# Performance work log

Hardware: AMD Instinct MI355X
Metric: run time of the kernel (lower is better)

The kernel has to match this reference:

```python
import jax, jax.numpy as jnp
import numpy as np

D = 1024
H = 16
HD = D // H

def setup_inputs() -> dict:
    key = jax.random.key(0)
    ks = jax.random.split(key, 6)
    tokens = jax.random.normal(ks[0], (2, 2048, D), dtype=jnp.float32)
    # LayerNorm params
    ln_gamma = jnp.ones((D,), dtype=jnp.float32)
    ln_beta = jnp.zeros((D,), dtype=jnp.float32)
    # qkv Linear (no bias): torch Linear weight is [3D, D]; store as [D, 3D] for x @ W
    w_qkv = jax.random.normal(ks[1], (D, 3 * D), dtype=jnp.float32) / np.sqrt(D)
    # output projection with bias
    w_proj = jax.random.normal(ks[2], (D, D), dtype=jnp.float32) / np.sqrt(D)
    b_proj = jax.random.normal(ks[3], (D,), dtype=jnp.float32) * 0.01
    return {"tokens": tokens, "ln_gamma": ln_gamma, "ln_beta": ln_beta,
            "w_qkv": w_qkv, "w_proj": w_proj, "b_proj": b_proj}

def reference(tokens, ln_gamma, ln_beta, w_qkv, w_proj, b_proj):
    B, S, _ = tokens.shape
    res = tokens
    # LayerNorm (eps=1e-5, torch default)
    mu = jnp.mean(tokens, axis=-1, keepdims=True)
    var = jnp.var(tokens, axis=-1, keepdims=True)
    x = (tokens - mu) * jax.lax.rsqrt(var + 1e-5) * ln_gamma + ln_beta
    # QKV projection -> [B, S, 3, H, HD] -> q,k,v each [B, H, S, HD]
    qkv = (x @ w_qkv).reshape(B, S, 3, H, HD)
    qkv = jnp.transpose(qkv, (2, 0, 3, 1, 4))
    q, k, v = qkv[0], qkv[1], qkv[2]
    scale = HD ** -0.5
    scores = jnp.einsum('bhsd,bhtd->bhst', q, k) * scale  # [B,H,S,S]
    attn = jax.nn.softmax(scores, axis=-1)
    dots = jnp.einsum('bhst,bhtd->bhsd', attn, v)          # [B,H,S,HD]
    dots = jnp.transpose(dots, (0, 2, 1, 3)).reshape(B, S, D)
    out = dots @ w_proj + b_proj
    return out + res
```

## Files before the change

### kernel.cpp

```cpp
#include <hip/hip_runtime.h>

typedef __bf16 bf16x8 __attribute__((ext_vector_type(8)));
typedef __bf16 bf16x4 __attribute__((ext_vector_type(4)));
typedef float f32x4 __attribute__((ext_vector_type(4)));
typedef unsigned short us8 __attribute__((ext_vector_type(8)));

__device__ __forceinline__ unsigned short f2bf(float f) {
  unsigned int u = __builtin_bit_cast(unsigned int, f);
  u += 0x7FFFu + ((u >> 16) & 1u);
  return (unsigned short)(u >> 16);
}
__device__ __forceinline__ float bf2f(unsigned short s) {
  return __builtin_bit_cast(float, (unsigned int)s << 16);
}

__device__ __forceinline__ void load_lds16(const void* g, void* l) {
  __builtin_amdgcn_global_load_lds(
      (const __attribute__((address_space(1))) unsigned int*)g,
      (__attribute__((address_space(3))) unsigned int*)l, 16, 0, 0);
}

#define MFMA16(a, b, c) __builtin_amdgcn_mfma_f32_16x16x32_bf16(a, b, c, 0, 0, 0)

constexpr int Dm = 1024, Ss = 2048;

__global__ __launch_bounds__(256) void ln_kernel(
    const float* __restrict__ x, const float* __restrict__ gamma,
    const float* __restrict__ beta, unsigned short* __restrict__ out) {
  const int row = blockIdx.x;
  const int t = threadIdx.x;
  const float4 v = reinterpret_cast<const float4*>(x + (size_t)row * Dm)[t];
  float s = v.x + v.y + v.z + v.w;
  float ss = v.x * v.x + v.y * v.y + v.z * v.z + v.w * v.w;
#pragma unroll
  for (int off = 1; off < 64; off <<= 1) {
    s += __shfl_xor(s, off);
    ss += __shfl_xor(ss, off);
  }
  __shared__ float sb[8];
  const int lane = t & 63, wid = t >> 6;
  if (lane == 0) { sb[wid] = s; sb[4 + wid] = ss; }
  __syncthreads();
  s = sb[0] + sb[1] + sb[2] + sb[3];
  ss = sb[4] + sb[5] + sb[6] + sb[7];
  const float mu = s * (1.0f / Dm);
  const float var = ss * (1.0f / Dm) - mu * mu;
  const float rs = rsqrtf(var + 1e-5f);
  const float4 g = reinterpret_cast<const float4*>(gamma)[t];
  const float4 bt = reinterpret_cast<const float4*>(beta)[t];
  ushort4 pack;
  pack.x = f2bf((v.x - mu) * rs * g.x + bt.x);
  pack.y = f2bf((v.y - mu) * rs * g.y + bt.y);
  pack.z = f2bf((v.z - mu) * rs * g.z + bt.z);
  pack.w = f2bf((v.w - mu) * rs * g.w + bt.w);
  reinterpret_cast<ushort4*>(out + (size_t)row * Dm)[t] = pack;
}

__global__ __launch_bounds__(256) void transpose_kernel(
    const float* __restrict__ in, unsigned short* __restrict__ out, int K, int N) {
  __shared__ float tile[32][33];
  const int tx = threadIdx.x & 31, ty = threadIdx.x >> 5;
  const int n0 = blockIdx.x * 32, k0 = blockIdx.y * 32;
#pragma unroll
  for (int i = 0; i < 4; i++)
    tile[ty + i * 8][tx] = in[(size_t)(k0 + ty + i * 8) * N + n0 + tx];
  __syncthreads();
#pragma unroll
  for (int i = 0; i < 4; i++)
    out[(size_t)(n0 + ty + i * 8) * K + k0 + tx] = f2bf(tile[tx][ty + i * 8]);
}

template <int EPI, int BN>
__global__ __launch_bounds__(256) void gemm_kernel(
    const unsigned short* __restrict__ A, const unsigned short* __restrict__ Bt,
    int N, int K, int nbx, unsigned short* __restrict__ Cbf,
    unsigned short* __restrict__ vt, float* __restrict__ Cf,
    const float* __restrict__ bias, const float* __restrict__ resid) {
  __shared__ unsigned short Al[128 * 64];
  __shared__ unsigned short Bl[BN * 64];
  constexpr int NJ = BN / 32;
  const int tid = threadIdx.x;
  const int lane = tid & 63, wid = tid >> 6;
  const int l15 = lane & 15, lg = lane >> 4;
  const int wm = wid >> 1, wn = wid & 1;
  const int cpx = gridDim.x >> 3;
  const int lb = (blockIdx.x & 7) * cpx + (blockIdx.x >> 3);
  const int bx = lb % nbx, by = lb / nbx;
  const int bm = by * 128, bn = bx * BN;
  const int r8 = lane >> 3;
  const int swz = ((lane & 7) * 16) ^ (r8 << 4);
  const char* Ab = (const char*)A;
  const char* Bb = (const char*)Bt;
  f32x4 acc[4][NJ] = {};
  for (int k0 = 0; k0 < K; k0 += 64) {
    __syncthreads();
#pragma unroll
    for (int p = 0; p < 4; p++) {
      const int row = p * 32 + wid * 8 + r8;
      load_lds16(Ab + ((size_t)(bm + row) * K + k0) * 2 + swz,
                 (char*)Al + p * 4096 + wid * 1024);
    }
#pragma unroll
    for (int p = 0; p < BN / 32; p++) {
      const int row = p * 32 + wid * 8 + r8;
      load_lds16(Bb + ((size_t)(bn + row) * K + k0) * 2 + swz,
                 (char*)Bl + p * 4096 + wid * 1024);
    }
    __syncthreads();
#pragma unroll
    for (int kk = 0; kk < 2; kk++) {
      bf16x8 af[4], bfr[NJ];
#pragma unroll
      for (int mi = 0; mi < 4; mi++) {
        const int row = wm * 64 + mi * 16 + l15;
        af[mi] = *(const bf16x8*)((const char*)Al + row * 128 +
                                  ((kk * 64 + lg * 16) ^ ((row & 7) << 4)));
      }
#pragma unroll
      for (int nj = 0; nj < NJ; nj++) {
        const int row = wn * (BN / 2) + nj * 16 + l15;
        bfr[nj] = *(const bf16x8*)((const char*)Bl + row * 128 +
                                   ((kk * 64 + lg * 16) ^ ((row & 7) << 4)));
      }
#pragma unroll
      for (int mi = 0; mi < 4; mi++)
#pragma unroll
        for (int nj = 0; nj < NJ; nj++)
          acc[mi][nj] = MFMA16(af[mi], bfr[nj], acc[mi][nj]);
    }
  }
#pragma unroll
  for (int mi = 0; mi < 4; mi++)
#pragma unroll
    for (int nj = 0; nj < NJ; nj++) {
      const int m = bm + wm * 64 + mi * 16 + lg * 4;
      const int n = bn + wn * (BN / 2) + nj * 16 + l15;
      if (EPI == 0) {
        if (n < 2048) {
          const float sc = (n < 1024) ? 0.180336880f : 1.0f;
#pragma unroll
          for (int r = 0; r < 4; r++)
            Cbf[(size_t)(m + r) * N + n] = f2bf(acc[mi][nj][r] * sc);
        } else {
          const int h = (n - 2048) >> 6, hd = (n - 2048) & 63;
          const int bq = m >> 11, s = m & 2047;
          bf16x4 o;
#pragma unroll
          for (int r = 0; r < 4; r++) o[r] = (__bf16)acc[mi][nj][r];
          *(bf16x4*)(vt + ((size_t)((bq << 4) + h) * 64 + hd) * 2048 + s) = o;
        }
      } else {
#pragma unroll
        for (int r = 0; r < 4; r++) {
          const size_t idx = (size_t)(m + r) * N + n;
          Cf[idx] = acc[mi][nj][r] + bias[n] + resid[idx];
        }
      }
    }
}

__global__ __launch_bounds__(512) void attn_kernel(
    const unsigned short* __restrict__ qkv, const unsigned short* __restrict__ vt,
    unsigned short* part0, unsigned short* part1, float* __restrict__ ml) {
  __shared__ unsigned short Kb[2][64 * 64];
  __shared__ unsigned short Vb[2][64 * 64];
  __shared__ unsigned short Pl[8][32][64];
  const int tid = threadIdx.x, lane = tid & 63, wid = tid >> 6;
  const int l15 = lane & 15, lg = lane >> 4;
  const int lb = (blockIdx.x & 7) * 64 + (blockIdx.x >> 3);
  const int bh = lb >> 4, qt = (lb >> 1) & 7, half = lb & 1;
  const int b = bh >> 4, h = bh & 15;
  const int q0 = qt * 256 + wid * 32;
  const unsigned short* qbase = qkv + (size_t)(b * Ss) * 3072 + h * 64;
  const char* kbase = (const char*)(qkv + (size_t)(b * Ss) * 3072 + 1024 + h * 64);
  const char* vbase = (const char*)(vt + (size_t)bh * 64 * Ss);

  bf16x8 qf[2][2];
#pragma unroll
  for (int qj = 0; qj < 2; qj++)
#pragma unroll
    for (int kk = 0; kk < 2; kk++)
      qf[qj][kk] = *reinterpret_cast<const bf16x8*>(
          &qbase[(size_t)(q0 + qj * 16 + l15) * 3072 + kk * 32 + lg * 8]);

  f32x4 accT[4][2] = {};
  float psum[2] = {0.f, 0.f};

  const int srow = lane >> 3;
  const int swz = ((lane & 7) * 16) ^ (srow << 4);

#define STAGE(bufi, t0v)                                                          \
  {                                                                               \
    load_lds16(kbase + (size_t)((t0v) + wid * 8 + srow) * 6144 + swz,             \
               (char*)&Kb[bufi][0] + wid * 1024);                                 \
    load_lds16(vbase + (size_t)(wid * 8 + srow) * 4096 + (size_t)(t0v) * 2 + swz, \
               (char*)&Vb[bufi][0] + wid * 1024);                                 \
  }

  const int t0base = half * 1024;
  STAGE(0, t0base);

  for (int itr = 0; itr < 16; itr++) {
    const int cur = itr & 1;
    asm volatile("s_waitcnt vmcnt(0)" ::: "memory");
    __builtin_amdgcn_s_barrier();
    if (itr + 1 < 16) STAGE(cur ^ 1, t0base + (itr + 1) * 64);

    const char* kcur = (const char*)&Kb[cur][0];
    const char* vcur = (const char*)&Vb[cur][0];

    f32x4 accs[4][2] = {};
    __builtin_amdgcn_s_setprio(1);
#pragma unroll
    for (int kk = 0; kk < 2; kk++) {
      bf16x8 kf[4];
#pragma unroll
      for (int kvi = 0; kvi < 4; kvi++) {
        const int rk = kvi * 16 + l15;
        kf[kvi] = *(const bf16x8*)(kcur + rk * 128 +
                                   ((kk * 64 + lg * 16) ^ ((rk & 7) << 4)));
      }
#pragma unroll
      for (int kvi = 0; kvi < 4; kvi++)
#pragma unroll
        for (int qj = 0; qj < 2; qj++)
          accs[kvi][qj] = MFMA16(kf[kvi], qf[qj][kk], accs[kvi][qj]);
    }
    __builtin_amdgcn_s_setprio(0);

#pragma unroll
    for (int qj = 0; qj < 2; qj++) {
      const int prow = qj * 16 + l15;
      char* prl = (char*)&Pl[wid][prow][0];
      float ps = 0.f;
#pragma unroll
      for (int kvi = 0; kvi < 4; kvi++) {
        bf16x4 pk;
#pragma unroll
        for (int r = 0; r < 4; r++) {
          const float p = exp2f(accs[kvi][qj][r]);
          ps += p;
          pk[r] = (__bf16)p;
        }
        *(bf16x4*)(prl + ((kvi * 32 + lg * 8) ^ ((l15 & 7) << 4))) = pk;
      }
      psum[qj] += ps;
    }

    asm volatile("s_waitcnt lgkmcnt(0)" ::: "memory");
    __builtin_amdgcn_sched_barrier(0);

    __builtin_amdgcn_s_setprio(1);
#pragma unroll
    for (int kk2 = 0; kk2 < 2; kk2++) {
      bf16x8 pf[2], vf[4];
#pragma unroll
      for (int qj = 0; qj < 2; qj++)
        pf[qj] = *(const bf16x8*)((const char*)&Pl[wid][qj * 16 + l15][0] +
                                  ((kk2 * 64 + lg * 16) ^ ((l15 & 7) << 4)));
#pragma unroll
      for (int nj = 0; nj < 4; nj++) {
        const int rv = nj * 16 + l15;
        vf[nj] = *(const bf16x8*)(vcur + rv * 128 +
                                  ((kk2 * 64 + lg * 16) ^ ((rv & 7) << 4)));
      }
#pragma unroll
      for (int nj = 0; nj < 4; nj++)
#pragma unroll
        for (int qj = 0; qj < 2; qj++)
          accT[nj][qj] = MFMA16(vf[nj], pf[qj], accT[nj][qj]);
    }
    __builtin_amdgcn_s_setprio(0);
  }

#pragma unroll
  for (int qj = 0; qj < 2; qj++) {
    psum[qj] += __shfl_xor(psum[qj], 16);
    psum[qj] += __shfl_xor(psum[qj], 32);
  }
  unsigned short* pout = half ? part1 : part0;
#pragma unroll
  for (int qj = 0; qj < 2; qj++) {
    const float rl = 1.0f / psum[qj];
    const int q = q0 + qj * 16 + l15;
#pragma unroll
    for (int nj = 0; nj < 4; nj++) {
      bf16x4 o;
#pragma unroll
      for (int r = 0; r < 4; r++) o[r] = (__bf16)(accT[nj][qj][r] * rl);
      *(bf16x4*)(pout + (size_t)(b * Ss + q) * Dm + h * 64 + nj * 16 + lg * 4) = o;
    }
  }
  if (lg == 0) {
#pragma unroll
    for (int qj = 0; qj < 2; qj++)
      ml[half * 65536 + bh * 2048 + q0 + qj * 16 + l15] = psum[qj];
  }
}

__global__ __launch_bounds__(256) void combine_kernel(
    const unsigned short* p0, const unsigned short* __restrict__ p1,
    const float* __restrict__ ml, unsigned short* dots) {
  const int t = blockIdx.x * 256 + threadIdx.x;
  const int hd8 = t & 7;
  const int h = (t >> 3) & 15;
  const int row = t >> 7;
  const int b = row >> 11, s = row & 2047;
  const int bh = b * 16 + h;
  const float w0 = ml[bh * 2048 + s];
  const float w1 = ml[65536 + bh * 2048 + s];
  const float inv = 1.0f / (w0 + w1);
  const size_t off = (size_t)row * 1024 + h * 64 + hd8 * 8;
  const us8 a = *(const us8*)(p0 + off);
  const us8 c = *(const us8*)(p1 + off);
  us8 o;
#pragma unroll
  for (int j = 0; j < 8; j++)
    o[j] = f2bf((bf2f(a[j]) * w0 + bf2f(c[j]) * w1) * inv);
  *(us8*)(dots + off) = o;
}

extern "C" void kernel_launch(void* const* d_in, const int* in_sizes, int n_in,
                              void* d_out, int out_size, void* d_ws, size_t ws_size,
                              hipStream_t stream) {
  const float* tokens = (const float*)d_in[0];
  const float* ln_g = (const float*)d_in[1];
  const float* ln_b = (const float*)d_in[2];
  const float* w_qkv = (const float*)d_in[3];
  const float* w_proj = (const float*)d_in[4];
  const float* b_proj = (const float*)d_in[5];
  float* out = (float*)d_out;

  char* ws = (char*)d_ws;
  unsigned short* x_bf = (unsigned short*)(ws);
  unsigned short* wqkvT = (unsigned short*)(ws + 8388608);
  unsigned short* wprojT = (unsigned short*)(ws + 14680064);
  unsigned short* qkvraw = (unsigned short*)(ws + 16777216);
  unsigned short* vt = (unsigned short*)(ws + 41943040);
  unsigned short* part1 = (unsigned short*)(ws + 50331648);
  float* ml = (float*)(ws + 58720256);
  unsigned short* dots = x_bf;

  ln_kernel<<<4096, 256, 0, stream>>>(tokens, ln_g, ln_b, x_bf);
  transpose_kernel<<<dim3(3072 / 32, 1024 / 32), 256, 0, stream>>>(w_qkv, wqkvT, 1024, 3072);
  transpose_kernel<<<dim3(1024 / 32, 1024 / 32), 256, 0, stream>>>(w_proj, wprojT, 1024, 1024);
  gemm_kernel<0, 128><<<768, 256, 0, stream>>>(
      x_bf, wqkvT, 3072, 1024, 24, qkvraw, vt, nullptr, nullptr, nullptr);
  attn_kernel<<<512, 512, 0, stream>>>(qkvraw, vt, dots, part1, ml);
  combine_kernel<<<2048, 256, 0, stream>>>(dots, part1, ml, dots);
  gemm_kernel<1, 64><<<512, 256, 0, stream>>>(
      dots, wprojT, 1024, 1024, 16, nullptr, nullptr, out, b_proj, tokens);
}
```

Measured before the change: 137.5 us.

## Replace QKV GEMM with 256x256-tile 8-wave kernel using deep LDS pipelining

Adds a dedicated QKV projection GEMM with 256x256 output tiles, 512 threads and 128 KB of dynamic LDS. It overlaps global-to-LDS direct loads with MFMA compute through a hand-scheduled double-buffered pipeline of barriers and waitcnts. The goal is higher data reuse per tile and less load latency on the K loop than the previous 128x128 kernel. The risks are that only 192 blocks launch, so some CUs on the 256-CU device sit idle, and the hand-written barrier and waitcnt schedule is fragile.

```diff
diff --git a/kernel.cpp b/kernel.cpp
--- a/kernel.cpp
+++ b/kernel.cpp
@@ -68,6 +68,119 @@
 #pragma unroll
   for (int i = 0; i < 4; i++)
     out[(size_t)(n0 + ty + i * 8) * K + k0 + tx] = f2bf(tile[tx][ty + i * 8]);
+}
+
+__global__ __launch_bounds__(512) void gemm256_kernel(
+    const unsigned short* __restrict__ A, const unsigned short* __restrict__ Bt,
+    unsigned short* __restrict__ Cbf, unsigned short* __restrict__ vt) {
+  extern __shared__ char lds[];
+  const int tid = threadIdx.x;
+  const int lane = tid & 63, wid = tid >> 6;
+  const int l15 = lane & 15, lg = lane >> 4;
+  const int wr = wid >> 2, wc = wid & 3;
+  const int lb = (blockIdx.x & 7) * 24 + (blockIdx.x >> 3);
+  const int bx = lb % 12, by = lb / 12;
+  const int bm = by * 256, bn = bx * 256;
+  const int sswz = ((lane & 3) * 16) ^ (((lane >> 2) & 3) << 4);
+  const char* Asrc = (const char*)A + (size_t)(bm + wid * 32 + (lane >> 2)) * 2048 + sswz;
+  const char* Bsrc = (const char*)Bt + (size_t)(bn + wid * 32 + (lane >> 2)) * 2048 + sswz;
+  const int rdsz = ((lg * 16) ^ ((l15 & 3) << 4));
+
+#define STG_A(kk_, bufT, tile_)                                                 \
+  if ((tile_) < 16) {                                                           \
+    _Pragma("unroll") for (int c = 0; c < 2; c++)                               \
+      load_lds16(Asrc + (size_t)(c * 16) * 2048 + (tile_) * 128 + (kk_) * 64,   \
+                 lds + ((bufT) * 2 + (kk_)) * 16384 + wid * 2048 + c * 1024);   \
+  }
+#define STG_B(kk_, bufT, tile_)                                                 \
+  if ((tile_) < 16) {                                                           \
+    _Pragma("unroll") for (int c = 0; c < 2; c++)                               \
+      load_lds16(Bsrc + (size_t)(c * 16) * 2048 + (tile_) * 128 + (kk_) * 64,   \
+                 lds + 65536 + ((bufT) * 2 + (kk_)) * 16384 + wid * 2048 +      \
+                     c * 1024);                                                 \
+  }
+#define DS_A(buf_, kk_)                                                         \
+  _Pragma("unroll") for (int mi = 0; mi < 8; mi++) {                            \
+    const int r = wr * 128 + mi * 16 + l15;                                     \
+    af[mi] = *(const bf16x8*)(lds + ((buf_) * 2 + (kk_)) * 16384 + r * 64 + rdsz); \
+  }
+#define DS_B(buf_, kk_, nh_)                                                    \
+  _Pragma("unroll") for (int nj = 0; nj < 2; nj++) {                            \
+    const int r = wc * 64 + (nh_) * 32 + nj * 16 + l15;                         \
+    bfr[nj] = *(const bf16x8*)(lds + 65536 + ((buf_) * 2 + (kk_)) * 16384 +     \
+                               r * 64 + rdsz);                                  \
+  }
+#define MM(nh_)                                                                 \
+  __builtin_amdgcn_s_setprio(1);                                                \
+  _Pragma("unroll") for (int mi = 0; mi < 8; mi++)                              \
+      _Pragma("unroll") for (int nj = 0; nj < 2; nj++)                          \
+          acc[mi][(nh_) * 2 + nj] = MFMA16(af[mi], bfr[nj], acc[mi][(nh_) * 2 + nj]); \
+  __builtin_amdgcn_s_setprio(0);
+#define GBAR __builtin_amdgcn_s_barrier()
+#define LGKM0 asm volatile("s_waitcnt lgkmcnt(0)" ::: "memory")
+
+  f32x4 acc[8][4] = {};
+
+  STG_A(0, 0, 0); STG_B(0, 0, 0); STG_A(1, 0, 0); STG_B(1, 0, 0);
+  STG_A(0, 1, 1); STG_B(0, 1, 1); STG_A(1, 1, 1);
+  asm volatile("s_waitcnt vmcnt(6)" ::: "memory");
+  GBAR;
+
+  for (int i = 0; i < 8; ++i) {
+    const int t2 = 2 * i + 2, t3 = 2 * i + 3;
+    const bool last = (i == 7);
+    bf16x8 af[8], bfr[2];
+    DS_A(0, 0); DS_B(0, 0, 0); STG_B(1, 1, 2 * i + 1);
+    GBAR; LGKM0; MM(0); GBAR;
+    DS_B(0, 0, 1); STG_A(0, 0, t2);
+    GBAR; LGKM0; MM(1); GBAR;
+    DS_A(0, 1); DS_B(0, 1, 0); STG_B(0, 0, t2);
+    GBAR; LGKM0; MM(0); GBAR;
+    DS_B(0, 1, 1); STG_A(1, 0, t2);
+    GBAR; LGKM0; MM(1);
+    if (last) asm volatile("s_waitcnt vmcnt(0)" ::: "memory");
+    else      asm volatile("s_waitcnt vmcnt(6)" ::: "memory");
+    GBAR;
+    DS_A(1, 0); DS_B(1, 0, 0); STG_B(1, 0, t2);
+    GBAR; LGKM0; MM(0); GBAR;
+    DS_B(1, 0, 1); STG_A(0, 1, t3);
+    GBAR; LGKM0; MM(1); GBAR;
+    DS_A(1, 1); DS_B(1, 1, 0); STG_B(0, 1, t3);
+    GBAR; LGKM0; MM(0); GBAR;
+    DS_B(1, 1, 1); STG_A(1, 1, t3);
+    GBAR; LGKM0; MM(1);
+    if (last) asm volatile("s_waitcnt vmcnt(0)" ::: "memory");
+    else      asm volatile("s_waitcnt vmcnt(6)" ::: "memory");
+    GBAR;
+  }
+
+#pragma unroll
+  for (int mi = 0; mi < 8; mi++)
+#pragma unroll
+    for (int nj = 0; nj < 4; nj++) {
+      const int m = bm + wr * 128 + mi * 16 + lg * 4;
+      const int n = bn + wc * 64 + nj * 16 + l15;
+      if (n < 2048) {
+        const float sc = (n < 1024) ? 0.180336880f : 1.0f;
+#pragma unroll
+        for (int r = 0; r < 4; r++)
+          Cbf[(size_t)(m + r) * 3072 + n] = f2bf(acc[mi][nj][r] * sc);
+      } else {
+        const int h = (n - 2048) >> 6, hd = (n - 2048) & 63;
+        const int bq = m >> 11, s = m & 2047;
+        bf16x4 o;
+#pragma unroll
+        for (int r = 0; r < 4; r++) o[r] = (__bf16)acc[mi][nj][r];
+        *(bf16x4*)(vt + ((size_t)((bq << 4) + h) * 64 + hd) * 2048 + s) = o;
+      }
+    }
+#undef STG_A
+#undef STG_B
+#undef DS_A
+#undef DS_B
+#undef MM
+#undef GBAR
+#undef LGKM0
 }
 
 template <int EPI, int BN>
@@ -341,11 +454,13 @@
   float* ml = (float*)(ws + 58720256);
   unsigned short* dots = x_bf;
 
+  hipFuncSetAttribute((const void*)gemm256_kernel,
+                      hipFuncAttributeMaxDynamicSharedMemorySize, 131072);
+
   ln_kernel<<<4096, 256, 0, stream>>>(tokens, ln_g, ln_b, x_bf);
   transpose_kernel<<<dim3(3072 / 32, 1024 / 32), 256, 0, stream>>>(w_qkv, wqkvT, 1024, 3072);
   transpose_kernel<<<dim3(1024 / 32, 1024 / 32), 256, 0, stream>>>(w_proj, wprojT, 1024, 1024);
-  gemm_kernel<0, 128><<<768, 256, 0, stream>>>(
-      x_bf, wqkvT, 3072, 1024, 24, qkvraw, vt, nullptr, nullptr, nullptr);
+  gemm256_kernel<<<192, 512, 131072, stream>>>(x_bf, wqkvT, qkvraw, vt);
   attn_kernel<<<512, 512, 0, stream>>>(qkvraw, vt, dots, part1, ml);
   combine_kernel<<<2048, 256, 0, stream>>>(dots, part1, ml, dots);
   gemm_kernel<1, 64><<<512, 256, 0, stream>>>(
```

Measured after the change: 134.3 us. -2.3%, faster.
